# Kernel optimization log

Measured on AMD Instinct MI355X. Metric: run time of the kernel, lower is better.

## Reference

```python
import jax, jax.numpy as jnp
import numpy as np

EPSILON = 1e-36


def setup_inputs() -> dict:
    key = jax.random.key(0)
    k1, k2, k3, k4 = jax.random.split(key, 4)
    n, in_dim, out_dim = 8192, 128, 128
    x = jax.random.normal(k1, (n, in_dim), dtype=jnp.float32)
    # xavier-uniform-like scale for W_real
    limit = float(np.sqrt(6.0 / (in_dim + out_dim)))
    W_real = jax.random.uniform(k2, (in_dim, out_dim), dtype=jnp.float32, minval=-limit, maxval=limit)
    W_imag = jax.random.uniform(k3, (in_dim, out_dim), dtype=jnp.float32, minval=-0.1, maxval=0.1)
    G = jax.random.uniform(k4, (in_dim, out_dim), dtype=jnp.float32, minval=0.0, maxval=1.0)
    return {"x": x, "W_real": W_real, "W_imag": W_imag, "G": G}


def reference(x, W_real, W_imag, G):
    Gc = jnp.clip(G, 0.0, 1.0)                                   # (i,o)
    # R: (n,i,o) = |x| gated toward 1 by (1-G)
    R = (jnp.abs(x) + EPSILON)[:, :, None] * Gc[None] + (1.0 - Gc)[None]
    # K: pi where x<0, gated by G
    K = jnp.pi * (x < 0).astype(x.dtype)[:, :, None] * Gc[None]  # (n,i,o)
    logR = jnp.log(R)
    A = jnp.einsum('nio,io->no', logR, W_real) - jnp.einsum('nio,io->no', K, W_imag)
    B = jnp.einsum('nio,io->no', logR, W_imag) + jnp.einsum('nio,io->no', K, W_real)
    return jnp.exp(A) * jnp.cos(B)
```

## Files before the change

kernel.cpp:

```cpp
#include <hip/hip_runtime.h>
#include <math.h>


#define NROWS 8192
#define DIM   128
#define RPB   8
#define NT    512
#define IQ    32
#define PI_F  3.14159265358979323846f
#define LN2_F 0.69314718055994530942f

typedef float v2f __attribute__((ext_vector_type(2)));

static __device__ __forceinline__ v2f vfma2(v2f a, v2f b, v2f c) {
    return __builtin_elementwise_fma(a, b, c);
}

__global__ __launch_bounds__(256) void prep_w(
    const float* __restrict__ Wr, const float* __restrict__ Wi,
    const float* __restrict__ G, float4* __restrict__ wq)
{
    int t = blockIdx.x * 256 + threadIdx.x;
    if (t < DIM * DIM) {
        float g  = fminf(fmaxf(G[t], 0.0f), 1.0f);
        wq[t] = make_float4(LN2_F * Wr[t], LN2_F * Wi[t], g, g * (1.0f / LN2_F));
    }
}

template <bool PACKED>
__global__ __launch_bounds__(NT, 8) void main_kernel(
    const float* __restrict__ x, const float4* __restrict__ wq,
    const float* __restrict__ Wr, const float* __restrict__ Wi,
    const float* __restrict__ G, float* __restrict__ out)
{
    __shared__ float sbuf[4 * RPB * DIM];
    float* am1p = sbuf;
    float* psp  = sbuf + DIM * RPB;

    const int tid   = threadIdx.x;
    const int o     = tid & (DIM - 1);
    const int q     = tid >> 7;
    const int nbase = blockIdx.x * RPB;
    const float* xb = x + (size_t)nbase * DIM;

    {
        float2 v = ((const float2*)xb)[tid];
        int e = tid * 2;
        int i = e & (DIM - 1), r = e >> 7;
        am1p[i * RPB + r]       = fabsf(v.x) - 1.0f;
        am1p[(i + 1) * RPB + r] = fabsf(v.y) - 1.0f;
        psp[i * RPB + r]        = (v.x < 0.0f) ? PI_F : 0.0f;
        psp[(i + 1) * RPB + r]  = (v.y < 0.0f) ? PI_F : 0.0f;
    }
    __syncthreads();

    v2f accA[4], accB[4];
#pragma unroll
    for (int p = 0; p < 4; ++p) { accA[p] = (v2f){0.f, 0.f}; accB[p] = (v2f){0.f, 0.f}; }

    const int ibase = q * IQ;
    const float4* wqp = PACKED ? (wq + ibase * DIM + o) : nullptr;

    float4 wcur;
    if (PACKED) wcur = wqp[0];

#pragma unroll 2
    for (int ii = 0; ii < IQ; ++ii) {
        const int i = ibase + ii;
        float wrl, wil, g, gq;
        float4 wnxt;
        if (PACKED) {
            wnxt = wqp[((ii + 1) & (IQ - 1)) * DIM];
            wrl = wcur.x; wil = wcur.y; g = wcur.z; gq = wcur.w;
        } else {
            g   = fminf(fmaxf(G[i * DIM + o], 0.0f), 1.0f);
            wrl = LN2_F * Wr[i * DIM + o];
            wil = LN2_F * Wi[i * DIM + o];
            gq  = g * (1.0f / LN2_F);
        }
        const float ngwi = -gq * wil;
        const float gwr  =  gq * wrl;
        const v2f gg2   = {g, g};
        const v2f wrl2  = {wrl, wrl};
        const v2f wil2  = {wil, wil};
        const v2f ngwi2 = {ngwi, ngwi};
        const v2f gwr2  = {gwr, gwr};
        const v2f one2  = {1.0f, 1.0f};

        const float4* a4 = (const float4*)(am1p + i * RPB);
        const float4* p4 = (const float4*)(psp  + i * RPB);
        float4 a03 = a4[0], a47 = a4[1];
        float4 s03 = p4[0], s47 = p4[1];

#define ROWPAIR(mx, my, sx, sy, idx)                                        \
        do {                                                                \
            v2f t2 = vfma2((v2f){mx, my}, gg2, one2);                       \
            v2f l2 = { __log2f(t2.x), __log2f(t2.y) };                      \
            v2f s2 = {sx, sy};                                              \
            accA[idx] = vfma2(l2, wrl2, vfma2(s2, ngwi2, accA[idx]));       \
            accB[idx] = vfma2(l2, wil2, vfma2(s2, gwr2,  accB[idx]));       \
        } while (0)

        ROWPAIR(a03.x, a03.y, s03.x, s03.y, 0);
        ROWPAIR(a03.z, a03.w, s03.z, s03.w, 1);
        ROWPAIR(a47.x, a47.y, s47.x, s47.y, 2);
        ROWPAIR(a47.z, a47.w, s47.z, s47.w, 3);
#undef ROWPAIR

        if (PACKED) wcur = wnxt;
    }

    float* pP = sbuf;
    const int c = tid * 2;
    const int r = c >> 7, oo = c & (DIM - 1);

    __syncthreads();
#pragma unroll
    for (int p = 0; p < 4; ++p) {
        pP[q * (RPB * DIM) + (2 * p) * DIM + o]     = accA[p].x;
        pP[q * (RPB * DIM) + (2 * p + 1) * DIM + o] = accA[p].y;
    }
    __syncthreads();
    v2f A = {0.f, 0.f};
#pragma unroll
    for (int qq = 0; qq < 4; ++qq)
        A += *(const v2f*)&pP[qq * (RPB * DIM) + r * DIM + oo];
    __syncthreads();
#pragma unroll
    for (int p = 0; p < 4; ++p) {
        pP[q * (RPB * DIM) + (2 * p) * DIM + o]     = accB[p].x;
        pP[q * (RPB * DIM) + (2 * p + 1) * DIM + o] = accB[p].y;
    }
    __syncthreads();
    v2f B = {0.f, 0.f};
#pragma unroll
    for (int qq = 0; qq < 4; ++qq)
        B += *(const v2f*)&pP[qq * (RPB * DIM) + r * DIM + oo];

    float2 res;
    res.x = __expf(A.x) * __cosf(B.x);
    res.y = __expf(A.y) * __cosf(B.y);
    *(float2*)&out[(size_t)(nbase + r) * DIM + oo] = res;
}

extern "C" void kernel_launch(void* const* d_in, const int* in_sizes, int n_in,
                              void* d_out, int out_size, void* d_ws, size_t ws_size,
                              hipStream_t stream) {
    const float* x  = (const float*)d_in[0];
    const float* Wr = (const float*)d_in[1];
    const float* Wi = (const float*)d_in[2];
    const float* G  = (const float*)d_in[3];
    float* out = (float*)d_out;

    const size_t wq_bytes = (size_t)DIM * DIM * sizeof(float4);
    if (ws_size >= wq_bytes) {
        float4* wq = (float4*)d_ws;
        prep_w<<<(DIM * DIM + 255) / 256, 256, 0, stream>>>(Wr, Wi, G, wq);
        main_kernel<true><<<NROWS / RPB, NT, 0, stream>>>(x, wq,
                                                          nullptr, nullptr, nullptr, out);
    } else {
        main_kernel<false><<<NROWS / RPB, NT, 0, stream>>>(x, nullptr,
                                                           Wr, Wi, G, out);
    }
}
```

Before: 85.57 us.

## Precompute transposed x features in prep kernel and stream them from global memory

The prep kernel now also converts x into a per-block transposed layout holding |x|-1 and the sign-phase term, interleaved 16 floats per input index, written to workspace. The main kernel's packed path reads these with wave-uniform float4 loads that are prefetched one iteration ahead, instead of staging them in shared memory. This removes the LDS staging step and its initial barrier. The cost is an extra global write and read of about 8 MB of transformed data, plus a larger prep launch.

```diff
diff --git a/kernel.cpp b/kernel.cpp
--- a/kernel.cpp
+++ b/kernel.cpp
@@ -16,105 +16,157 @@
     return __builtin_elementwise_fma(a, b, c);
 }
 
-__global__ __launch_bounds__(256) void prep_w(
+__global__ __launch_bounds__(256) void prep(
+    const float* __restrict__ x,
     const float* __restrict__ Wr, const float* __restrict__ Wi,
-    const float* __restrict__ G, float4* __restrict__ wq)
+    const float* __restrict__ G,
+    float4* __restrict__ wq, float* __restrict__ xt)
 {
-    int t = blockIdx.x * 256 + threadIdx.x;
-    if (t < DIM * DIM) {
+    const int b = blockIdx.x;
+    if (b < 64) {
+        int t = b * 256 + threadIdx.x;
         float g  = fminf(fmaxf(G[t], 0.0f), 1.0f);
         wq[t] = make_float4(LN2_F * Wr[t], LN2_F * Wi[t], g, g * (1.0f / LN2_F));
+    } else {
+        const int db = b - 64;
+        const float4* xb = (const float4*)(x + (size_t)db * RPB * DIM);
+        float4 v = xb[threadIdx.x];
+        int e = threadIdx.x * 4;
+        int i = e & (DIM - 1), r = e >> 7;
+        float* op = xt + (size_t)db * (DIM * 16);
+        float vv[4] = {v.x, v.y, v.z, v.w};
+#pragma unroll
+        for (int k = 0; k < 4; ++k) {
+            op[(i + k) * 16 + r]     = fabsf(vv[k]) - 1.0f;
+            op[(i + k) * 16 + 8 + r] = (vv[k] < 0.0f) ? PI_F : 0.0f;
+        }
     }
 }
 
 template <bool PACKED>
 __global__ __launch_bounds__(NT, 8) void main_kernel(
     const float* __restrict__ x, const float4* __restrict__ wq,
+    const float* __restrict__ xt,
     const float* __restrict__ Wr, const float* __restrict__ Wi,
     const float* __restrict__ G, float* __restrict__ out)
 {
     __shared__ float sbuf[4 * RPB * DIM];
-    float* am1p = sbuf;
-    float* psp  = sbuf + DIM * RPB;
 
     const int tid   = threadIdx.x;
     const int o     = tid & (DIM - 1);
     const int q     = tid >> 7;
     const int nbase = blockIdx.x * RPB;
-    const float* xb = x + (size_t)nbase * DIM;
-
-    {
-        float2 v = ((const float2*)xb)[tid];
-        int e = tid * 2;
-        int i = e & (DIM - 1), r = e >> 7;
-        am1p[i * RPB + r]       = fabsf(v.x) - 1.0f;
-        am1p[(i + 1) * RPB + r] = fabsf(v.y) - 1.0f;
-        psp[i * RPB + r]        = (v.x < 0.0f) ? PI_F : 0.0f;
-        psp[(i + 1) * RPB + r]  = (v.y < 0.0f) ? PI_F : 0.0f;
-    }
-    __syncthreads();
 
     v2f accA[4], accB[4];
 #pragma unroll
     for (int p = 0; p < 4; ++p) { accA[p] = (v2f){0.f, 0.f}; accB[p] = (v2f){0.f, 0.f}; }
 
     const int ibase = q * IQ;
-    const float4* wqp = PACKED ? (wq + ibase * DIM + o) : nullptr;
-
-    float4 wcur;
-    if (PACKED) wcur = wqp[0];
+
+    if constexpr (PACKED) {
+        const float4* wqp = wq + ibase * DIM + o;
+        const int qu = __builtin_amdgcn_readfirstlane(q);
+        const float4* xtb = (const float4*)(xt + (size_t)blockIdx.x * (DIM * 16))
+                            + qu * (IQ * 4);
+
+        float4 wcur = wqp[0];
+        float4 aLc = xtb[0], aHc = xtb[1], sLc = xtb[2], sHc = xtb[3];
 
 #pragma unroll 2
-    for (int ii = 0; ii < IQ; ++ii) {
-        const int i = ibase + ii;
-        float wrl, wil, g, gq;
-        float4 wnxt;
-        if (PACKED) {
-            wnxt = wqp[((ii + 1) & (IQ - 1)) * DIM];
-            wrl = wcur.x; wil = wcur.y; g = wcur.z; gq = wcur.w;
-        } else {
-            g   = fminf(fmaxf(G[i * DIM + o], 0.0f), 1.0f);
-            wrl = LN2_F * Wr[i * DIM + o];
-            wil = LN2_F * Wi[i * DIM + o];
-            gq  = g * (1.0f / LN2_F);
-        }
-        const float ngwi = -gq * wil;
-        const float gwr  =  gq * wrl;
-        const v2f gg2   = {g, g};
-        const v2f wrl2  = {wrl, wrl};
-        const v2f wil2  = {wil, wil};
-        const v2f ngwi2 = {ngwi, ngwi};
-        const v2f gwr2  = {gwr, gwr};
-        const v2f one2  = {1.0f, 1.0f};
-
-        const float4* a4 = (const float4*)(am1p + i * RPB);
-        const float4* p4 = (const float4*)(psp  + i * RPB);
-        float4 a03 = a4[0], a47 = a4[1];
-        float4 s03 = p4[0], s47 = p4[1];
+        for (int ii = 0; ii < IQ; ++ii) {
+            const int nx = (ii + 1) & (IQ - 1);
+            float4 wnxt = wqp[nx * DIM];
+            float4 aLn = xtb[nx * 4 + 0];
+            float4 aHn = xtb[nx * 4 + 1];
+            float4 sLn = xtb[nx * 4 + 2];
+            float4 sHn = xtb[nx * 4 + 3];
+
+            const float wrl = wcur.x, wil = wcur.y, g = wcur.z, gq = wcur.w;
+            const float ngwi = -gq * wil;
+            const float gwr  =  gq * wrl;
+            const v2f gg2   = {g, g};
+            const v2f wrl2  = {wrl, wrl};
+            const v2f wil2  = {wil, wil};
+            const v2f ngwi2 = {ngwi, ngwi};
+            const v2f gwr2  = {gwr, gwr};
+            const v2f one2  = {1.0f, 1.0f};
+
+#define ROWPAIR(ax, ay, sx, sy, idx)                                        \
+            do {                                                            \
+                v2f t2 = vfma2((v2f){ax, ay}, gg2, one2);                   \
+                v2f l2 = { __log2f(t2.x), __log2f(t2.y) };                  \
+                v2f s2 = {sx, sy};                                          \
+                accA[idx] = vfma2(l2, wrl2, vfma2(s2, ngwi2, accA[idx]));   \
+                accB[idx] = vfma2(l2, wil2, vfma2(s2, gwr2,  accB[idx]));   \
+            } while (0)
+
+            ROWPAIR(aLc.x, aLc.y, sLc.x, sLc.y, 0);
+            ROWPAIR(aLc.z, aLc.w, sLc.z, sLc.w, 1);
+            ROWPAIR(aHc.x, aHc.y, sHc.x, sHc.y, 2);
+            ROWPAIR(aHc.z, aHc.w, sHc.z, sHc.w, 3);
+#undef ROWPAIR
+
+            wcur = wnxt;
+            aLc = aLn; aHc = aHn; sLc = sLn; sHc = sHn;
+        }
+    } else {
+        float* am1p = sbuf;
+        float* psp  = sbuf + DIM * RPB;
+        {
+            const float* xb = x + (size_t)nbase * DIM;
+            float2 v = ((const float2*)xb)[tid];
+            int e = tid * 2;
+            int i = e & (DIM - 1), r = e >> 7;
+            am1p[i * RPB + r]       = fabsf(v.x) - 1.0f;
+            am1p[(i + 1) * RPB + r] = fabsf(v.y) - 1.0f;
+            psp[i * RPB + r]        = (v.x < 0.0f) ? PI_F : 0.0f;
+            psp[(i + 1) * RPB + r]  = (v.y < 0.0f) ? PI_F : 0.0f;
+        }
+        __syncthreads();
+
+#pragma unroll 2
+        for (int ii = 0; ii < IQ; ++ii) {
+            const int i = ibase + ii;
+            float g   = fminf(fmaxf(G[i * DIM + o], 0.0f), 1.0f);
+            float wrl = LN2_F * Wr[i * DIM + o];
+            float wil = LN2_F * Wi[i * DIM + o];
+            float gq  = g * (1.0f / LN2_F);
+            const float ngwi = -gq * wil;
+            const float gwr  =  gq * wrl;
+            const v2f gg2   = {g, g};
+            const v2f wrl2  = {wrl, wrl};
+            const v2f wil2  = {wil, wil};
+            const v2f ngwi2 = {ngwi, ngwi};
+            const v2f gwr2  = {gwr, gwr};
+            const v2f one2  = {1.0f, 1.0f};
+
+            const float4* a4 = (const float4*)(am1p + i * RPB);
+            const float4* p4 = (const float4*)(psp  + i * RPB);
+            float4 a03 = a4[0], a47 = a4[1];
+            float4 s03 = p4[0], s47 = p4[1];
 
 #define ROWPAIR(mx, my, sx, sy, idx)                                        \
-        do {                                                                \
-            v2f t2 = vfma2((v2f){mx, my}, gg2, one2);                       \
-            v2f l2 = { __log2f(t2.x), __log2f(t2.y) };                      \
-            v2f s2 = {sx, sy};                                              \
-            accA[idx] = vfma2(l2, wrl2, vfma2(s2, ngwi2, accA[idx]));       \
-            accB[idx] = vfma2(l2, wil2, vfma2(s2, gwr2,  accB[idx]));       \
-        } while (0)
-
-        ROWPAIR(a03.x, a03.y, s03.x, s03.y, 0);
-        ROWPAIR(a03.z, a03.w, s03.z, s03.w, 1);
-        ROWPAIR(a47.x, a47.y, s47.x, s47.y, 2);
-        ROWPAIR(a47.z, a47.w, s47.z, s47.w, 3);
+            do {                                                            \
+                v2f t2 = vfma2((v2f){mx, my}, gg2, one2);                   \
+                v2f l2 = { __log2f(t2.x), __log2f(t2.y) };                  \
+                v2f s2 = {sx, sy};                                          \
+                accA[idx] = vfma2(l2, wrl2, vfma2(s2, ngwi2, accA[idx]));   \
+                accB[idx] = vfma2(l2, wil2, vfma2(s2, gwr2,  accB[idx]));   \
+            } while (0)
+
+            ROWPAIR(a03.x, a03.y, s03.x, s03.y, 0);
+            ROWPAIR(a03.z, a03.w, s03.z, s03.w, 1);
+            ROWPAIR(a47.x, a47.y, s47.x, s47.y, 2);
+            ROWPAIR(a47.z, a47.w, s47.z, s47.w, 3);
 #undef ROWPAIR
-
-        if (PACKED) wcur = wnxt;
+        }
     }
 
     float* pP = sbuf;
     const int c = tid * 2;
     const int r = c >> 7, oo = c & (DIM - 1);
 
-    __syncthreads();
+    if constexpr (!PACKED) __syncthreads();
 #pragma unroll
     for (int p = 0; p < 4; ++p) {
         pP[q * (RPB * DIM) + (2 * p) * DIM + o]     = accA[p].x;
@@ -153,13 +205,15 @@
     float* out = (float*)d_out;
 
     const size_t wq_bytes = (size_t)DIM * DIM * sizeof(float4);
-    if (ws_size >= wq_bytes) {
+    const size_t xt_bytes = (size_t)(NROWS / RPB) * DIM * 16 * sizeof(float);
+    if (ws_size >= wq_bytes + xt_bytes) {
         float4* wq = (float4*)d_ws;
-        prep_w<<<(DIM * DIM + 255) / 256, 256, 0, stream>>>(Wr, Wi, G, wq);
-        main_kernel<true><<<NROWS / RPB, NT, 0, stream>>>(x, wq,
+        float*  xt = (float*)((char*)d_ws + wq_bytes);
+        prep<<<64 + NROWS / RPB, 256, 0, stream>>>(x, Wr, Wi, G, wq, xt);
+        main_kernel<true><<<NROWS / RPB, NT, 0, stream>>>(x, wq, xt,
                                                           nullptr, nullptr, nullptr, out);
     } else {
-        main_kernel<false><<<NROWS / RPB, NT, 0, stream>>>(x, nullptr,
+        main_kernel<false><<<NROWS / RPB, NT, 0, stream>>>(x, nullptr, nullptr,
                                                            Wr, Wi, G, out);
     }
 }
```

Result: slower. 90.99 us (+6.3%).

## Drop weight-packing prep kernel and read raw weights in main kernel

Applied to the files above, without the earlier changes.

Removes the separate prep_w launch that packed LN2-scaled weights and clamped gate into a float4 workspace. The main kernel now loads Wr, Wi and G directly each iteration and recomputes the scaling, with unroll raised to 4 and the launch-bounds occupancy hint lowered from 8 to 4. This saves one kernel launch and the workspace round trip, at the cost of three scalar loads plus a few extra ALU ops per iteration and no explicit prefetch.

```diff
diff --git a/kernel.cpp b/kernel.cpp
--- a/kernel.cpp
+++ b/kernel.cpp
@@ -16,20 +16,8 @@
     return __builtin_elementwise_fma(a, b, c);
 }
 
-__global__ __launch_bounds__(256) void prep_w(
-    const float* __restrict__ Wr, const float* __restrict__ Wi,
-    const float* __restrict__ G, float4* __restrict__ wq)
-{
-    int t = blockIdx.x * 256 + threadIdx.x;
-    if (t < DIM * DIM) {
-        float g  = fminf(fmaxf(G[t], 0.0f), 1.0f);
-        wq[t] = make_float4(LN2_F * Wr[t], LN2_F * Wi[t], g, g * (1.0f / LN2_F));
-    }
-}
-
-template <bool PACKED>
-__global__ __launch_bounds__(NT, 8) void main_kernel(
-    const float* __restrict__ x, const float4* __restrict__ wq,
+__global__ __launch_bounds__(NT, 4) void main_kernel(
+    const float* __restrict__ x,
     const float* __restrict__ Wr, const float* __restrict__ Wi,
     const float* __restrict__ G, float* __restrict__ out)
 {
@@ -41,9 +29,9 @@
     const int o     = tid & (DIM - 1);
     const int q     = tid >> 7;
     const int nbase = blockIdx.x * RPB;
-    const float* xb = x + (size_t)nbase * DIM;
 
     {
+        const float* xb = x + (size_t)nbase * DIM;
         float2 v = ((const float2*)xb)[tid];
         int e = tid * 2;
         int i = e & (DIM - 1), r = e >> 7;
@@ -59,27 +47,19 @@
     for (int p = 0; p < 4; ++p) { accA[p] = (v2f){0.f, 0.f}; accB[p] = (v2f){0.f, 0.f}; }
 
     const int ibase = q * IQ;
-    const float4* wqp = PACKED ? (wq + ibase * DIM + o) : nullptr;
+    const int wo    = ibase * DIM + o;
 
-    float4 wcur;
-    if (PACKED) wcur = wqp[0];
+#pragma unroll 4
+    for (int ii = 0; ii < IQ; ++ii) {
+        const int i  = ibase + ii;
+        const int wi_idx = wo + ii * DIM;
 
-#pragma unroll 2
-    for (int ii = 0; ii < IQ; ++ii) {
-        const int i = ibase + ii;
-        float wrl, wil, g, gq;
-        float4 wnxt;
-        if (PACKED) {
-            wnxt = wqp[((ii + 1) & (IQ - 1)) * DIM];
-            wrl = wcur.x; wil = wcur.y; g = wcur.z; gq = wcur.w;
-        } else {
-            g   = fminf(fmaxf(G[i * DIM + o], 0.0f), 1.0f);
-            wrl = LN2_F * Wr[i * DIM + o];
-            wil = LN2_F * Wi[i * DIM + o];
-            gq  = g * (1.0f / LN2_F);
-        }
-        const float ngwi = -gq * wil;
-        const float gwr  =  gq * wrl;
+        float g   = fminf(fmaxf(G[wi_idx], 0.0f), 1.0f);
+        float wrl = LN2_F * Wr[wi_idx];
+        float wil = LN2_F * Wi[wi_idx];
+
+        const float ngwi = -g * (wil * (1.0f / LN2_F));
+        const float gwr  =  g * (wrl * (1.0f / LN2_F));
         const v2f gg2   = {g, g};
         const v2f wrl2  = {wrl, wrl};
         const v2f wil2  = {wil, wil};
@@ -106,8 +86,6 @@
         ROWPAIR(a47.x, a47.y, s47.x, s47.y, 2);
         ROWPAIR(a47.z, a47.w, s47.z, s47.w, 3);
 #undef ROWPAIR
-
-        if (PACKED) wcur = wnxt;
     }
 
     float* pP = sbuf;
@@ -152,14 +130,7 @@
     const float* G  = (const float*)d_in[3];
     float* out = (float*)d_out;
 
-    const size_t wq_bytes = (size_t)DIM * DIM * sizeof(float4);
-    if (ws_size >= wq_bytes) {
-        float4* wq = (float4*)d_ws;
-        prep_w<<<(DIM * DIM + 255) / 256, 256, 0, stream>>>(Wr, Wi, G, wq);
-        main_kernel<true><<<NROWS / RPB, NT, 0, stream>>>(x, wq,
-                                                          nullptr, nullptr, nullptr, out);
-    } else {
-        main_kernel<false><<<NROWS / RPB, NT, 0, stream>>>(x, nullptr,
-                                                           Wr, Wi, G, out);
-    }
+    (void)d_ws; (void)ws_size;
+
+    main_kernel<<<NROWS / RPB, NT, 0, stream>>>(x, Wr, Wi, G, out);
 }
```

Measured after the change: 88.55 us. +3.5%, slower.
